# Performance work log

Hardware: AMD Instinct MI355X
Metric: run time of the kernel (lower is better)

The kernel has to match this reference:

```python
import jax, jax.numpy as jnp
import numpy as np

N_NODES = 50000
N_EDGES = 800000
HIDDEN = 128


def setup_inputs() -> dict:
    key = jax.random.key(0)
    ks = jax.random.split(key, 8)
    z = jax.random.normal(ks[0], (N_NODES, HIDDEN), dtype=jnp.float32)
    weights = jax.random.normal(ks[1], (N_EDGES, 1), dtype=jnp.float32)
    sources = jax.random.randint(ks[2], (N_EDGES,), 0, N_NODES)
    dests = jax.random.randint(ks[3], (N_EDGES,), 0, N_NODES)
    # Linear params (stored [in, out]); scale ~ 1/sqrt(fan_in) like torch default
    in_m = 2 * HIDDEN + 1
    in_u = 2 * HIDDEN
    Wm = jax.random.uniform(ks[4], (in_m, HIDDEN), dtype=jnp.float32, minval=-1.0, maxval=1.0) / np.sqrt(in_m)
    bm = jax.random.uniform(ks[5], (HIDDEN,), dtype=jnp.float32, minval=-1.0, maxval=1.0) / np.sqrt(in_m)
    Wu = jax.random.uniform(ks[6], (in_u, HIDDEN), dtype=jnp.float32, minval=-1.0, maxval=1.0) / np.sqrt(in_u)
    bu = jax.random.uniform(ks[7], (HIDDEN,), dtype=jnp.float32, minval=-1.0, maxval=1.0) / np.sqrt(in_u)
    return {"z": z, "weights": weights, "sources": sources, "dests": dests,
            "Wm": Wm, "bm": bm, "Wu": Wu, "bu": bu}


def reference(z, weights, sources, dests, Wm, bm, Wu, bu):
    n = z.shape[0]
    # gather + concat message input: [E, 2d+1]
    inp = jnp.concatenate([z[dests], z[sources], weights], axis=1)
    messages = inp @ Wm + bm                      # [E, d]
    # scatter_reduce amax over destination nodes; empty segments -> -inf
    m = jax.ops.segment_max(messages, dests, num_segments=n)
    m = jnp.where(jnp.isneginf(m), jnp.zeros_like(m), m)
    h = jnp.concatenate([z, m], axis=1) @ Wu + bu  # [N, d]
    return h
```

## Files before the change

kernel.cpp:

```cpp
#include <hip/hip_runtime.h>
#include <math.h>

#define HIDDEN 128
#define PAD_DEG 64
#define NPART 8
#define CHUNK 2048

typedef __attribute__((ext_vector_type(8))) _Float16 f16x8;
typedef __attribute__((ext_vector_type(4))) float f32x4;
typedef __attribute__((ext_vector_type(2))) _Float16 h2;

__device__ inline unsigned short f2h(float x) {
    _Float16 h = (_Float16)x;
    return __builtin_bit_cast(unsigned short, h);
}
__device__ inline float h2f(unsigned short u) {
    return (float)__builtin_bit_cast(_Float16, u);
}
__device__ inline float h2f_lo(unsigned int u) { return h2f((unsigned short)(u & 0xffff)); }
__device__ inline float h2f_hi(unsigned int u) { return h2f((unsigned short)(u >> 16)); }
__device__ inline h2 hmax2(h2 a, h2 b) {
    h2 r;
    r[0] = a[0] > b[0] ? a[0] : b[0];
    r[1] = a[1] > b[1] ? a[1] : b[1];
    return r;
}

__global__ void prep_kernel(const float* __restrict__ Wm, const float* __restrict__ Wu,
                            unsigned short* __restrict__ WmT0, unsigned short* __restrict__ WmT1,
                            unsigned short* __restrict__ WuT, float* __restrict__ wlast,
                            int* __restrict__ counts, int n) {
    int t = blockIdx.x * blockDim.x + threadIdx.x;
    if (t < 16384) {
        int nn = t >> 7, k = t & 127;
        WmT0[t] = f2h(Wm[k * 128 + nn]);
    } else if (t < 32768) {
        int s = t - 16384;
        int nn = s >> 7, k = s & 127;
        WmT1[s] = f2h(Wm[(128 + k) * 128 + nn]);
    } else if (t < 65536) {
        int s = t - 32768;
        int nn = s >> 8, k = s & 255;
        WuT[s] = f2h(Wu[k * 128 + nn]);
    } else if (t < 65664) {
        int i = t - 65536;
        wlast[i] = Wm[256 * 128 + i];
    } else if (t < 65664 + n) {
        counts[t - 65664] = 0;
    }
}

__global__ __launch_bounds__(256) void gemm_msg(const float* __restrict__ Z,
                                                const unsigned short* __restrict__ WmT0,
                                                const unsigned short* __restrict__ WmT1,
                                                unsigned short* __restrict__ P1h,
                                                unsigned short* __restrict__ P2h,
                                                int n) {
    __shared__ unsigned short As[64][136];
    __shared__ unsigned short Bs[128][136];

    const int m0 = blockIdx.x * 64;
    const int tid = threadIdx.x;
    const int wave = tid >> 6, lane = tid & 63;
    const int l15 = lane & 15, q = lane >> 4;
    const int wrow = wave * 16;

#pragma unroll
    for (int i = 0; i < 4; ++i) {
        int f = tid + i * 256;
        int row = f >> 4, c8 = f & 15;
        int gr = min(m0 + row, n - 1);
        const float4* src = (const float4*)&Z[(size_t)gr * 128 + c8 * 8];
        float4 a = src[0], b = src[1];
        f16x8 hv;
        hv[0] = (_Float16)a.x; hv[1] = (_Float16)a.y; hv[2] = (_Float16)a.z; hv[3] = (_Float16)a.w;
        hv[4] = (_Float16)b.x; hv[5] = (_Float16)b.y; hv[6] = (_Float16)b.z; hv[7] = (_Float16)b.w;
        *(f16x8*)&As[row][c8 * 8] = hv;
    }

    for (int part = 0; part < 2; ++part) {
        const float4* bsrc = (const float4*)(part == 0 ? WmT0 : WmT1);
        unsigned short* Out = part == 0 ? P1h : P2h;

#pragma unroll
        for (int i = 0; i < 8; ++i) {
            int f = tid + i * 256;
            int row = f >> 4, c4 = f & 15;
            *(float4*)&Bs[row][c4 * 8] = bsrc[row * 16 + c4];
        }
        __syncthreads();

        f32x4 acc[8];
#pragma unroll
        for (int nt = 0; nt < 8; ++nt) acc[nt] = (f32x4){0.f, 0.f, 0.f, 0.f};

#pragma unroll
        for (int ks = 0; ks < 4; ++ks) {
            int k0 = ks * 32;
            f16x8 a = *(const f16x8*)&As[wrow + l15][k0 + q * 8];
#pragma unroll
            for (int nt = 0; nt < 8; ++nt) {
                f16x8 b = *(const f16x8*)&Bs[nt * 16 + l15][k0 + q * 8];
                acc[nt] = __builtin_amdgcn_mfma_f32_16x16x32_f16(a, b, acc[nt], 0, 0, 0);
            }
        }

#pragma unroll
        for (int nt = 0; nt < 8; ++nt) {
#pragma unroll
            for (int r = 0; r < 4; ++r) {
                int row = m0 + wrow + q * 4 + r;
                if (row < n) Out[(size_t)row * 128 + nt * 16 + l15] = f2h(acc[nt][r]);
            }
        }
        __syncthreads();
    }
}

__global__ __launch_bounds__(256) void scatter_part(const int* __restrict__ dests,
                                                    const int* __restrict__ sources,
                                                    const float* __restrict__ weights,
                                                    int* __restrict__ counts,
                                                    unsigned int* __restrict__ edge_pk,
                                                    int E, int span, int n) {
    const int part = blockIdx.x & (NPART - 1);
    const int chunk = blockIdx.x >> 3;
    const int lo = part * span;
    const int hi = min(lo + span, n);
    const int base = chunk * CHUNK;

#pragma unroll
    for (int i = 0; i < CHUNK; i += 256) {
        int e = base + i + threadIdx.x;
        if (e < E) {
            int d = dests[e];
            if (d >= lo && d < hi) {
                int pos = atomicAdd(&counts[d], 1);
                if (pos < PAD_DEG) {
                    unsigned int pk = (unsigned int)(sources[e] & 0xffff) |
                                      ((unsigned int)f2h(weights[e]) << 16);
                    edge_pk[(size_t)d * PAD_DEG + pos] = pk;
                }
            }
        }
    }
}

__global__ __launch_bounds__(256) void segmax_kernel(const unsigned short* __restrict__ P1h,
                                                     const unsigned short* __restrict__ P2h,
                                                     const int* __restrict__ counts,
                                                     const unsigned int* __restrict__ edge_pk,
                                                     const float* __restrict__ wlast,
                                                     const float* __restrict__ bm,
                                                     unsigned short* __restrict__ Mh, int n) {
    const int wave = threadIdx.x >> 6;
    const int lane = threadIdx.x & 63;
    const int v = blockIdx.x * 4 + wave;
    if (v >= n) return;

    const int l16 = lane & 15;
    const int e4 = lane >> 4;
    const uint4* P2q = (const uint4*)P2h;
    const int cnt = min(counts[v], PAD_DEG);

    int pk = (lane < cnt) ? (int)edge_pk[(size_t)v * PAD_DEG + lane] : 0;

    float4 wfa = ((const float4*)wlast)[l16 * 2];
    float4 wfb = ((const float4*)wlast)[l16 * 2 + 1];
    h2 wl0, wl1, wl2, wl3;
    wl0[0] = (_Float16)wfa.x; wl0[1] = (_Float16)wfa.y;
    wl1[0] = (_Float16)wfa.z; wl1[1] = (_Float16)wfa.w;
    wl2[0] = (_Float16)wfb.x; wl2[1] = (_Float16)wfb.y;
    wl3[0] = (_Float16)wfb.z; wl3[1] = (_Float16)wfb.w;

    const h2 NEGINF = __builtin_bit_cast(h2, 0xFC00FC00u);
    h2 a0 = NEGINF, a1 = NEGINF, a2 = NEGINF, a3 = NEGINF;

    int j = 0;
    for (; j + 8 <= cnt; j += 8) {
        unsigned int pa = (unsigned int)__shfl(pk, j + e4);
        unsigned int pb = (unsigned int)__shfl(pk, j + 4 + e4);
        int sa = pa & 0xffff, sb = pb & 0xffff;
        uint4 ua = P2q[(size_t)sa * 16 + l16];
        uint4 ub = P2q[(size_t)sb * 16 + l16];
        h2 wva = __builtin_bit_cast(h2, (pa & 0xffff0000u) | (pa >> 16));
        h2 wvb = __builtin_bit_cast(h2, (pb & 0xffff0000u) | (pb >> 16));
        a0 = hmax2(a0, wva * wl0 + __builtin_bit_cast(h2, ua.x));
        a1 = hmax2(a1, wva * wl1 + __builtin_bit_cast(h2, ua.y));
        a2 = hmax2(a2, wva * wl2 + __builtin_bit_cast(h2, ua.z));
        a3 = hmax2(a3, wva * wl3 + __builtin_bit_cast(h2, ua.w));
        a0 = hmax2(a0, wvb * wl0 + __builtin_bit_cast(h2, ub.x));
        a1 = hmax2(a1, wvb * wl1 + __builtin_bit_cast(h2, ub.y));
        a2 = hmax2(a2, wvb * wl2 + __builtin_bit_cast(h2, ub.z));
        a3 = hmax2(a3, wvb * wl3 + __builtin_bit_cast(h2, ub.w));
    }
    for (; j < cnt; j += 4) {
        int idx = j + e4;
        bool valid = idx < cnt;
        unsigned int pa = (unsigned int)__shfl(pk, valid ? idx : 0);
        if (valid) {
            int sa = pa & 0xffff;
            uint4 ua = P2q[(size_t)sa * 16 + l16];
            h2 wva = __builtin_bit_cast(h2, (pa & 0xffff0000u) | (pa >> 16));
            a0 = hmax2(a0, wva * wl0 + __builtin_bit_cast(h2, ua.x));
            a1 = hmax2(a1, wva * wl1 + __builtin_bit_cast(h2, ua.y));
            a2 = hmax2(a2, wva * wl2 + __builtin_bit_cast(h2, ua.z));
            a3 = hmax2(a3, wva * wl3 + __builtin_bit_cast(h2, ua.w));
        }
    }

    a0 = hmax2(a0, __builtin_bit_cast(h2, __shfl_xor(__builtin_bit_cast(int, a0), 16)));
    a1 = hmax2(a1, __builtin_bit_cast(h2, __shfl_xor(__builtin_bit_cast(int, a1), 16)));
    a2 = hmax2(a2, __builtin_bit_cast(h2, __shfl_xor(__builtin_bit_cast(int, a2), 16)));
    a3 = hmax2(a3, __builtin_bit_cast(h2, __shfl_xor(__builtin_bit_cast(int, a3), 16)));
    a0 = hmax2(a0, __builtin_bit_cast(h2, __shfl_xor(__builtin_bit_cast(int, a0), 32)));
    a1 = hmax2(a1, __builtin_bit_cast(h2, __shfl_xor(__builtin_bit_cast(int, a1), 32)));
    a2 = hmax2(a2, __builtin_bit_cast(h2, __shfl_xor(__builtin_bit_cast(int, a2), 32)));
    a3 = hmax2(a3, __builtin_bit_cast(h2, __shfl_xor(__builtin_bit_cast(int, a3), 32)));

    if (e4 == 0) {
        uint4 o = make_uint4(0, 0, 0, 0);
        if (cnt > 0) {
            uint4 p1 = ((const uint4*)P1h)[(size_t)v * 16 + l16];
            float4 b0 = ((const float4*)bm)[l16 * 2];
            float4 b1 = ((const float4*)bm)[l16 * 2 + 1];
            float m0 = h2f_lo(p1.x) + b0.x + (float)a0[0];
            float m1 = h2f_hi(p1.x) + b0.y + (float)a0[1];
            float m2 = h2f_lo(p1.y) + b0.z + (float)a1[0];
            float m3 = h2f_hi(p1.y) + b0.w + (float)a1[1];
            float m4 = h2f_lo(p1.z) + b1.x + (float)a2[0];
            float m5 = h2f_hi(p1.z) + b1.y + (float)a2[1];
            float m6 = h2f_lo(p1.w) + b1.z + (float)a3[0];
            float m7 = h2f_hi(p1.w) + b1.w + (float)a3[1];
            o.x = (unsigned int)f2h(m0) | ((unsigned int)f2h(m1) << 16);
            o.y = (unsigned int)f2h(m2) | ((unsigned int)f2h(m3) << 16);
            o.z = (unsigned int)f2h(m4) | ((unsigned int)f2h(m5) << 16);
            o.w = (unsigned int)f2h(m6) | ((unsigned int)f2h(m7) << 16);
        } else {
            unsigned int zh = (unsigned int)f2h(0.f);
            unsigned int zz = zh | (zh << 16);
            o = make_uint4(zz, zz, zz, zz);
        }
        ((uint4*)Mh)[(size_t)v * 16 + l16] = o;
    }
}

__global__ __launch_bounds__(256) void gemm_out(const float* __restrict__ Z,
                                                const unsigned short* __restrict__ Mh,
                                                const unsigned short* __restrict__ WuT,
                                                const float* __restrict__ bu,
                                                float* __restrict__ H, int n) {
    __shared__ unsigned short As[64][136];
    __shared__ unsigned short Bs[128][136];

    const int m0 = blockIdx.x * 64;
    const int tid = threadIdx.x;
    const int wave = tid >> 6, lane = tid & 63;
    const int l15 = lane & 15, q = lane >> 4;
    const int wrow = wave * 16;

    f32x4 acc[8];
#pragma unroll
    for (int nt = 0; nt < 8; ++nt) acc[nt] = (f32x4){0.f, 0.f, 0.f, 0.f};

    for (int h = 0; h < 2; ++h) {
#pragma unroll
        for (int i = 0; i < 8; ++i) {
            int f = tid + i * 256;
            int row = f >> 4, c4 = f & 15;
            *(float4*)&Bs[row][c4 * 8] = ((const float4*)WuT)[row * 32 + h * 16 + c4];
        }
        if (h == 0) {
#pragma unroll
            for (int i = 0; i < 4; ++i) {
                int f = tid + i * 256;
                int row = f >> 4, c8 = f & 15;
                int gr = min(m0 + row, n - 1);
                const float4* src = (const float4*)&Z[(size_t)gr * 128 + c8 * 8];
                float4 a = src[0], b = src[1];
                f16x8 hv;
                hv[0] = (_Float16)a.x; hv[1] = (_Float16)a.y; hv[2] = (_Float16)a.z; hv[3] = (_Float16)a.w;
                hv[4] = (_Float16)b.x; hv[5] = (_Float16)b.y; hv[6] = (_Float16)b.z; hv[7] = (_Float16)b.w;
                *(f16x8*)&As[row][c8 * 8] = hv;
            }
        } else {
#pragma unroll
            for (int i = 0; i < 4; ++i) {
                int f = tid + i * 256;
                int row = f >> 4, c4 = f & 15;
                int gr = min(m0 + row, n - 1);
                *(float4*)&As[row][c4 * 8] = ((const float4*)&Mh[(size_t)gr * 128])[c4];
            }
        }
        __syncthreads();

#pragma unroll
        for (int ks = 0; ks < 4; ++ks) {
            int k0 = ks * 32;
            f16x8 a = *(const f16x8*)&As[wrow + l15][k0 + q * 8];
#pragma unroll
            for (int nt = 0; nt < 8; ++nt) {
                f16x8 b = *(const f16x8*)&Bs[nt * 16 + l15][k0 + q * 8];
                acc[nt] = __builtin_amdgcn_mfma_f32_16x16x32_f16(a, b, acc[nt], 0, 0, 0);
            }
        }
        __syncthreads();
    }

#pragma unroll
    for (int nt = 0; nt < 8; ++nt) {
        int col = nt * 16 + l15;
        float bias = bu[col];
#pragma unroll
        for (int r = 0; r < 4; ++r) {
            int row = m0 + wrow + q * 4 + r;
            if (row < n) H[(size_t)row * 128 + col] = acc[nt][r] + bias;
        }
    }
}

extern "C" void kernel_launch(void* const* d_in, const int* in_sizes, int n_in,
                              void* d_out, int out_size, void* d_ws, size_t ws_size,
                              hipStream_t stream) {
    const float* z = (const float*)d_in[0];
    const float* weights = (const float*)d_in[1];
    const int* sources = (const int*)d_in[2];
    const int* dests = (const int*)d_in[3];
    const float* Wm = (const float*)d_in[4];
    const float* bm = (const float*)d_in[5];
    const float* Wu = (const float*)d_in[6];
    const float* bu = (const float*)d_in[7];

    const int n = in_sizes[0] / HIDDEN;
    const int E = in_sizes[1];
    float* H = (float*)d_out;

    char* w = (char*)d_ws;
    auto alloc = [&](size_t bytes) { void* p = w; w += (bytes + 255) & ~(size_t)255; return p; };
    unsigned short* P1h = (unsigned short*)alloc((size_t)n * 128 * 2);
    unsigned short* Mh  = (unsigned short*)alloc((size_t)n * 128 * 2);
    unsigned short* WmT0 = (unsigned short*)alloc(16384 * 2);
    unsigned short* WmT1 = (unsigned short*)alloc(16384 * 2);
    unsigned short* WuT  = (unsigned short*)alloc(32768 * 2);
    float* wlast = (float*)alloc(128 * 4);
    int* counts  = (int*)alloc((size_t)n * 4);
    unsigned int* edge_pk = (unsigned int*)alloc((size_t)n * PAD_DEG * 4);

    unsigned short* P2h = (unsigned short*)d_out;

    const int mblocks = (n + 63) / 64;
    const int prep_threads = 65664 + n;
    const int span = (n + NPART - 1) / NPART;
    const int nchunks = (E + CHUNK - 1) / CHUNK;

    prep_kernel<<<(prep_threads + 255) / 256, 256, 0, stream>>>(Wm, Wu, WmT0, WmT1, WuT,
                                                                wlast, counts, n);
    gemm_msg<<<mblocks, 256, 0, stream>>>(z, WmT0, WmT1, P1h, P2h, n);
    scatter_part<<<nchunks * NPART, 256, 0, stream>>>(dests, sources, weights, counts,
                                                      edge_pk, E, span, n);
    segmax_kernel<<<(n + 3) / 4, 256, 0, stream>>>(P1h, P2h, counts, edge_pk,
                                                   wlast, bm, Mh, n);
    gemm_out<<<mblocks, 256, 0, stream>>>(z, Mh, WuT, bu, H, n);
}
```

Before: 191.1 us.

## Fold destination-side message projection into the update weights algebraically

Result: no change. 191.5 us (+0.2%).

```diff
diff --git a/kernel.cpp b/kernel.cpp
--- a/kernel.cpp
+++ b/kernel.cpp
@@ -27,9 +27,10 @@
 }
 
 __global__ void prep_kernel(const float* __restrict__ Wm, const float* __restrict__ Wu,
+                            const float* __restrict__ bm, const float* __restrict__ bu,
                             unsigned short* __restrict__ WmT0, unsigned short* __restrict__ WmT1,
-                            unsigned short* __restrict__ WuT, float* __restrict__ wlast,
-                            int* __restrict__ counts, int n) {
+                            unsigned short* __restrict__ WuT_fold, float* __restrict__ bfold,
+                            float* __restrict__ wlast, int* __restrict__ counts, int n) {
     int t = blockIdx.x * blockDim.x + threadIdx.x;
     if (t < 16384) {
         int nn = t >> 7, k = t & 127;
@@ -38,22 +39,33 @@
         int s = t - 16384;
         int nn = s >> 7, k = s & 127;
         WmT1[s] = f2h(Wm[(128 + k) * 128 + nn]);
+    } else if (t < 49152) {
+        int s = t - 32768;
+        int nn = s >> 7, k = s & 127;
+        WuT_fold[nn * 256 + 128 + k] = f2h(Wu[(128 + k) * 128 + nn]);
     } else if (t < 65536) {
-        int s = t - 32768;
-        int nn = s >> 8, k = s & 255;
-        WuT[s] = f2h(Wu[k * 128 + nn]);
+        int s = t - 49152;
+        int k = s >> 7, nn = s & 127;
+        float acc = Wu[k * 128 + nn];
+        for (int j = 0; j < 128; ++j)
+            acc = fmaf(Wm[k * 128 + j], Wu[(128 + j) * 128 + nn], acc);
+        WuT_fold[nn * 256 + k] = f2h(acc);
     } else if (t < 65664) {
         int i = t - 65536;
         wlast[i] = Wm[256 * 128 + i];
-    } else if (t < 65664 + n) {
-        counts[t - 65664] = 0;
+    } else if (t < 65792) {
+        int i = t - 65664;
+        float acc = bu[i];
+        for (int k = 0; k < 128; ++k)
+            acc = fmaf(bm[k], Wu[(128 + k) * 128 + i], acc);
+        bfold[i] = acc;
+    } else if (t < 65792 + n) {
+        counts[t - 65792] = 0;
     }
 }
 
 __global__ __launch_bounds__(256) void gemm_msg(const float* __restrict__ Z,
-                                                const unsigned short* __restrict__ WmT0,
                                                 const unsigned short* __restrict__ WmT1,
-                                                unsigned short* __restrict__ P1h,
                                                 unsigned short* __restrict__ P2h,
                                                 int n) {
     __shared__ unsigned short As[64][136];
@@ -77,43 +89,36 @@
         hv[4] = (_Float16)b.x; hv[5] = (_Float16)b.y; hv[6] = (_Float16)b.z; hv[7] = (_Float16)b.w;
         *(f16x8*)&As[row][c8 * 8] = hv;
     }
-
-    for (int part = 0; part < 2; ++part) {
-        const float4* bsrc = (const float4*)(part == 0 ? WmT0 : WmT1);
-        unsigned short* Out = part == 0 ? P1h : P2h;
-
-#pragma unroll
-        for (int i = 0; i < 8; ++i) {
-            int f = tid + i * 256;
-            int row = f >> 4, c4 = f & 15;
-            *(float4*)&Bs[row][c4 * 8] = bsrc[row * 16 + c4];
-        }
-        __syncthreads();
-
-        f32x4 acc[8];
-#pragma unroll
-        for (int nt = 0; nt < 8; ++nt) acc[nt] = (f32x4){0.f, 0.f, 0.f, 0.f};
-
-#pragma unroll
-        for (int ks = 0; ks < 4; ++ks) {
-            int k0 = ks * 32;
-            f16x8 a = *(const f16x8*)&As[wrow + l15][k0 + q * 8];
-#pragma unroll
-            for (int nt = 0; nt < 8; ++nt) {
-                f16x8 b = *(const f16x8*)&Bs[nt * 16 + l15][k0 + q * 8];
-                acc[nt] = __builtin_amdgcn_mfma_f32_16x16x32_f16(a, b, acc[nt], 0, 0, 0);
-            }
-        }
-
+#pragma unroll
+    for (int i = 0; i < 8; ++i) {
+        int f = tid + i * 256;
+        int row = f >> 4, c4 = f & 15;
+        *(float4*)&Bs[row][c4 * 8] = ((const float4*)WmT1)[row * 16 + c4];
+    }
+    __syncthreads();
+
+    f32x4 acc[8];
+#pragma unroll
+    for (int nt = 0; nt < 8; ++nt) acc[nt] = (f32x4){0.f, 0.f, 0.f, 0.f};
+
+#pragma unroll
+    for (int ks = 0; ks < 4; ++ks) {
+        int k0 = ks * 32;
+        f16x8 a = *(const f16x8*)&As[wrow + l15][k0 + q * 8];
 #pragma unroll
         for (int nt = 0; nt < 8; ++nt) {
-#pragma unroll
-            for (int r = 0; r < 4; ++r) {
-                int row = m0 + wrow + q * 4 + r;
-                if (row < n) Out[(size_t)row * 128 + nt * 16 + l15] = f2h(acc[nt][r]);
-            }
-        }
-        __syncthreads();
+            f16x8 b = *(const f16x8*)&Bs[nt * 16 + l15][k0 + q * 8];
+            acc[nt] = __builtin_amdgcn_mfma_f32_16x16x32_f16(a, b, acc[nt], 0, 0, 0);
+        }
+    }
+
+#pragma unroll
+    for (int nt = 0; nt < 8; ++nt) {
+#pragma unroll
+        for (int r = 0; r < 4; ++r) {
+            int row = m0 + wrow + q * 4 + r;
+            if (row < n) P2h[(size_t)row * 128 + nt * 16 + l15] = f2h(acc[nt][r]);
+        }
     }
 }
 
@@ -146,13 +151,14 @@
     }
 }
 
-__global__ __launch_bounds__(256) void segmax_kernel(const unsigned short* __restrict__ P1h,
+__global__ __launch_bounds__(256) void segmax_kernel(const float* __restrict__ Z,
                                                      const unsigned short* __restrict__ P2h,
                                                      const int* __restrict__ counts,
                                                      const unsigned int* __restrict__ edge_pk,
                                                      const float* __restrict__ wlast,
+                                                     const unsigned short* __restrict__ WmT0,
                                                      const float* __restrict__ bm,
-                                                     unsigned short* __restrict__ Mh, int n) {
+                                                     unsigned short* __restrict__ Sh, int n) {
     const int wave = threadIdx.x >> 6;
     const int lane = threadIdx.x & 63;
     const int v = blockIdx.x * 4 + wave;
@@ -219,36 +225,35 @@
     a3 = hmax2(a3, __builtin_bit_cast(h2, __shfl_xor(__builtin_bit_cast(int, a3), 32)));
 
     if (e4 == 0) {
-        uint4 o = make_uint4(0, 0, 0, 0);
+        uint4 o;
         if (cnt > 0) {
-            uint4 p1 = ((const uint4*)P1h)[(size_t)v * 16 + l16];
-            float4 b0 = ((const float4*)bm)[l16 * 2];
-            float4 b1 = ((const float4*)bm)[l16 * 2 + 1];
-            float m0 = h2f_lo(p1.x) + b0.x + (float)a0[0];
-            float m1 = h2f_hi(p1.x) + b0.y + (float)a0[1];
-            float m2 = h2f_lo(p1.y) + b0.z + (float)a1[0];
-            float m3 = h2f_hi(p1.y) + b0.w + (float)a1[1];
-            float m4 = h2f_lo(p1.z) + b1.x + (float)a2[0];
-            float m5 = h2f_hi(p1.z) + b1.y + (float)a2[1];
-            float m6 = h2f_lo(p1.w) + b1.z + (float)a3[0];
-            float m7 = h2f_hi(p1.w) + b1.w + (float)a3[1];
-            o.x = (unsigned int)f2h(m0) | ((unsigned int)f2h(m1) << 16);
-            o.y = (unsigned int)f2h(m2) | ((unsigned int)f2h(m3) << 16);
-            o.z = (unsigned int)f2h(m4) | ((unsigned int)f2h(m5) << 16);
-            o.w = (unsigned int)f2h(m6) | ((unsigned int)f2h(m7) << 16);
+            o.x = __builtin_bit_cast(unsigned int, a0);
+            o.y = __builtin_bit_cast(unsigned int, a1);
+            o.z = __builtin_bit_cast(unsigned int, a2);
+            o.w = __builtin_bit_cast(unsigned int, a3);
         } else {
-            unsigned int zh = (unsigned int)f2h(0.f);
-            unsigned int zz = zh | (zh << 16);
-            o = make_uint4(zz, zz, zz, zz);
-        }
-        ((uint4*)Mh)[(size_t)v * 16 + l16] = o;
+            float s[8];
+#pragma unroll
+            for (int d = 0; d < 8; ++d) s[d] = bm[l16 * 8 + d];
+            for (int k = 0; k < 128; ++k) {
+                float zk = Z[(size_t)v * 128 + k];
+#pragma unroll
+                for (int d = 0; d < 8; ++d)
+                    s[d] = fmaf(zk, h2f(WmT0[(l16 * 8 + d) * 128 + k]), s[d]);
+            }
+            o.x = (unsigned int)f2h(-s[0]) | ((unsigned int)f2h(-s[1]) << 16);
+            o.y = (unsigned int)f2h(-s[2]) | ((unsigned int)f2h(-s[3]) << 16);
+            o.z = (unsigned int)f2h(-s[4]) | ((unsigned int)f2h(-s[5]) << 16);
+            o.w = (unsigned int)f2h(-s[6]) | ((unsigned int)f2h(-s[7]) << 16);
+        }
+        ((uint4*)Sh)[(size_t)v * 16 + l16] = o;
     }
 }
 
 __global__ __launch_bounds__(256) void gemm_out(const float* __restrict__ Z,
-                                                const unsigned short* __restrict__ Mh,
-                                                const unsigned short* __restrict__ WuT,
-                                                const float* __restrict__ bu,
+                                                const unsigned short* __restrict__ Sh,
+                                                const unsigned short* __restrict__ WuT_fold,
+                                                const float* __restrict__ bfold,
                                                 float* __restrict__ H, int n) {
     __shared__ unsigned short As[64][136];
     __shared__ unsigned short Bs[128][136];
@@ -268,7 +273,7 @@
         for (int i = 0; i < 8; ++i) {
             int f = tid + i * 256;
             int row = f >> 4, c4 = f & 15;
-            *(float4*)&Bs[row][c4 * 8] = ((const float4*)WuT)[row * 32 + h * 16 + c4];
+            *(float4*)&Bs[row][c4 * 8] = ((const float4*)WuT_fold)[row * 32 + h * 16 + c4];
         }
         if (h == 0) {
 #pragma unroll
@@ -289,7 +294,7 @@
                 int f = tid + i * 256;
                 int row = f >> 4, c4 = f & 15;
                 int gr = min(m0 + row, n - 1);
-                *(float4*)&As[row][c4 * 8] = ((const float4*)&Mh[(size_t)gr * 128])[c4];
+                *(float4*)&As[row][c4 * 8] = ((const float4*)&Sh[(size_t)gr * 128])[c4];
             }
         }
         __syncthreads();
@@ -310,7 +315,7 @@
 #pragma unroll
     for (int nt = 0; nt < 8; ++nt) {
         int col = nt * 16 + l15;
-        float bias = bu[col];
+        float bias = bfold[col];
 #pragma unroll
         for (int r = 0; r < 4; ++r) {
             int row = m0 + wrow + q * 4 + r;
@@ -337,11 +342,11 @@
 
     char* w = (char*)d_ws;
     auto alloc = [&](size_t bytes) { void* p = w; w += (bytes + 255) & ~(size_t)255; return p; };
-    unsigned short* P1h = (unsigned short*)alloc((size_t)n * 128 * 2);
-    unsigned short* Mh  = (unsigned short*)alloc((size_t)n * 128 * 2);
+    unsigned short* Sh  = (unsigned short*)alloc((size_t)n * 128 * 2);
     unsigned short* WmT0 = (unsigned short*)alloc(16384 * 2);
     unsigned short* WmT1 = (unsigned short*)alloc(16384 * 2);
-    unsigned short* WuT  = (unsigned short*)alloc(32768 * 2);
+    unsigned short* WuT_fold = (unsigned short*)alloc(32768 * 2);
+    float* bfold = (float*)alloc(128 * 4);
     float* wlast = (float*)alloc(128 * 4);
     int* counts  = (int*)alloc((size_t)n * 4);
     unsigned int* edge_pk = (unsigned int*)alloc((size_t)n * PAD_DEG * 4);
@@ -349,16 +354,16 @@
     unsigned short* P2h = (unsigned short*)d_out;
 
     const int mblocks = (n + 63) / 64;
-    const int prep_threads = 65664 + n;
+    const int prep_threads = 65792 + n;
     const int span = (n + NPART - 1) / NPART;
     const int nchunks = (E + CHUNK - 1) / CHUNK;
 
-    prep_kernel<<<(prep_threads + 255) / 256, 256, 0, stream>>>(Wm, Wu, WmT0, WmT1, WuT,
-                                                                wlast, counts, n);
-    gemm_msg<<<mblocks, 256, 0, stream>>>(z, WmT0, WmT1, P1h, P2h, n);
+    prep_kernel<<<(prep_threads + 255) / 256, 256, 0, stream>>>(Wm, Wu, bm, bu, WmT0, WmT1,
+                                                                WuT_fold, bfold, wlast, counts, n);
+    gemm_msg<<<mblocks, 256, 0, stream>>>(z, WmT1, P2h, n);
     scatter_part<<<nchunks * NPART, 256, 0, stream>>>(dests, sources, weights, counts,
                                                       edge_pk, E, span, n);
-    segmax_kernel<<<(n + 3) / 4, 256, 0, stream>>>(P1h, P2h, counts, edge_pk,
-                                                   wlast, bm, Mh, n);
-    gemm_out<<<mblocks, 256, 0, stream>>>(z, Mh, WuT, bu, H, n);
-}
+    segmax_kernel<<<(n + 3) / 4, 256, 0, stream>>>(z, P2h, counts, edge_pk,
+                                                   wlast, WmT0, bm, Sh, n);
+    gemm_out<<<mblocks, 256, 0, stream>>>(z, Sh, WuT_fold, bfold, H, n);
+}
```
